# Kernel tuning notes

Measured on AMD Instinct MI355X. Metric: run time of the kernel, lower is better.

Reference implementation:

```python
import jax, jax.numpy as jnp
import numpy as np

SEQ = 8192
IN_DIM = 1024
HIDDEN_DIM = 2048
N_EXPERTS = 8
TOPK = 2


def setup_inputs() -> dict:
    key = jax.random.key(0)
    ks = jax.random.split(key, 6)
    scale = 0.02
    inp = jax.random.normal(ks[0], (SEQ, IN_DIM), jnp.float32)
    weights = jax.random.uniform(ks[1], (SEQ, TOPK), jnp.float32)
    selections = jax.random.randint(ks[2], (SEQ, TOPK), 0, N_EXPERTS, jnp.int32)
    up_proj = jax.random.normal(ks[3], (HIDDEN_DIM * N_EXPERTS, IN_DIM), jnp.float32) * scale
    gate_proj = jax.random.normal(ks[4], (HIDDEN_DIM * N_EXPERTS, IN_DIM), jnp.float32) * scale
    down_proj = jax.random.normal(ks[5], (HIDDEN_DIM * N_EXPERTS, IN_DIM), jnp.float32) * scale
    return {"inp": inp, "weights": weights, "up_proj": up_proj,
            "gate_proj": gate_proj, "down_proj": down_proj, "selections": selections}


def reference(inp, weights, up_proj, gate_proj, down_proj, selections):
    seq, in_dim = inp.shape
    topk = selections.shape[-1]
    # dispatch: replicate each token topk times -> (seq*topk, in_dim)
    x = jnp.broadcast_to(inp[:, None, :], (seq, topk, in_dim)).reshape(-1, in_dim)
    e_ids = selections.reshape(-1)  # (seq*topk,) expert id per dispatched token
    W_up = up_proj.reshape(N_EXPERTS, HIDDEN_DIM, in_dim)
    W_gate = gate_proj.reshape(N_EXPERTS, HIDDEN_DIM, in_dim)
    W_down = down_proj.reshape(N_EXPERTS, HIDDEN_DIM, in_dim)
    out = jnp.zeros_like(x)
    # grouped (block-sparse) GEMM: loop over the small fixed expert set,
    # masking tokens not routed to this expert (gelu(0)*0 = 0, so math matches).
    for e in range(N_EXPERTS):
        mask = (e_ids == e)[:, None]
        xe = jnp.where(mask, x, 0.0)
        h = xe @ W_up[e].T        # (seq*topk, hidden)
        g = xe @ W_gate[e].T      # (seq*topk, hidden)
        out = out + jnp.where(mask, (jax.nn.gelu(g) * h) @ W_down[e], 0.0)
    # combine: weighted sum over topk expert outputs per token
    return (out.reshape(seq, topk, in_dim) * weights[:, :, None]).sum(axis=1)
```

## Files before the change

kernel.cpp:

```cpp
#include <hip/hip_runtime.h>


#define SEQ 8192
#define IN_DIM 1024
#define HID 2048
#define NEXP 8
#define TOPK 2
#define NSLOT (SEQ * TOPK)

#define BM 128
#define BK 64
#define MAX_TILES 136
#define BM1 256
#define MAX_T1 72

typedef unsigned short ushort_t;
typedef __bf16 bf16x8 __attribute__((ext_vector_type(8)));
typedef float f32x4 __attribute__((ext_vector_type(4)));

__device__ __forceinline__ ushort_t f2bf(float f) {
    union { float f; unsigned u; } v;
    v.f = f;
    unsigned r = v.u + 0x7FFFu + ((v.u >> 16) & 1u);
    return (ushort_t)(r >> 16);
}

__device__ __forceinline__ float gelu_tanh(float x) {
    float u = 0.7978845608028654f * x * (1.0f + 0.044715f * x * x);
    return x / (1.0f + __expf(-2.0f * u));
}

__device__ __forceinline__ void async16(const void* g, void* l) {
    __builtin_amdgcn_global_load_lds(
        (const __attribute__((address_space(1))) unsigned int*)g,
        (__attribute__((address_space(3))) unsigned int*)l, 16, 0, 0);
}

__device__ __forceinline__ void wait8_barrier() {
    asm volatile("s_waitcnt vmcnt(8)\ns_barrier" ::: "memory");
}
__device__ __forceinline__ void wait0_barrier() {
    asm volatile("s_waitcnt vmcnt(0)\ns_barrier" ::: "memory");
}
__device__ __forceinline__ void lds_barrier() {
    asm volatile("s_waitcnt lgkmcnt(0)\ns_barrier" ::: "memory");
}

__global__ void cast_bf16_kernel(const float* __restrict__ in,
                                 ushort_t* __restrict__ out, int n) {
    int i = (blockIdx.x * blockDim.x + threadIdx.x) * 4;
    if (i >= n) return;
    float4 v = *(const float4*)(in + i);
    union { ushort_t u[4]; uint2 v; } o;
    o.u[0] = f2bf(v.x); o.u[1] = f2bf(v.y);
    o.u[2] = f2bf(v.z); o.u[3] = f2bf(v.w);
    *(uint2*)(out + i) = o.v;
}

__global__ void transpose_cast_kernel(const float* __restrict__ in,
                                      ushort_t* __restrict__ out) {
    __shared__ float tile[32][33];
    int e = blockIdx.z;
    int d0 = blockIdx.x * 32, h0 = blockIdx.y * 32;
    int tx = threadIdx.x & 31, ty = threadIdx.x >> 5;
    const float* src = in + (size_t)e * HID * IN_DIM;
    for (int j = 0; j < 32; j += 8)
        tile[ty + j][tx] = src[(size_t)(h0 + ty + j) * IN_DIM + d0 + tx];
    __syncthreads();
    ushort_t* dst = out + (size_t)e * IN_DIM * HID;
    for (int j = 0; j < 32; j += 8)
        dst[(size_t)(d0 + ty + j) * HID + h0 + tx] = f2bf(tile[tx][ty + j]);
}

__global__ void route_kernel(const int* __restrict__ sel,
                             const float* __restrict__ wts,
                             int* __restrict__ meta,
                             int* __restrict__ stok,
                             int* __restrict__ sinv) {
    __shared__ int lc[256][NEXP];
    __shared__ int tot[NEXP];
    __shared__ int s_off[NEXP + 1];
    int t = threadIdx.x;
    int cnt[NEXP];
#pragma unroll
    for (int e = 0; e < NEXP; e++) cnt[e] = 0;
    int base = t * (NSLOT / 256);
    for (int i = 0; i < NSLOT / 256; i++) cnt[sel[base + i]]++;
#pragma unroll
    for (int e = 0; e < NEXP; e++) lc[t][e] = cnt[e];
    __syncthreads();
    if (t < NEXP) {
        int run = 0;
        for (int i = 0; i < 256; i++) { int v = lc[i][t]; lc[i][t] = run; run += v; }
        tot[t] = run;
    }
    __syncthreads();
    if (t == 0) {
        int o = 0;
        for (int e = 0; e < NEXP; e++) { s_off[e] = o; o += tot[e]; }
        s_off[NEXP] = o;
        for (int e = 0; e <= NEXP; e++) meta[e] = s_off[e];
        int nt = 0;
        for (int e = 0; e < NEXP; e++) {
            int c = s_off[e + 1] - s_off[e];
            int m = (c + BM - 1) / BM;
            for (int i = 0; i < m; i++) { meta[32 + 2 * nt] = e; meta[33 + 2 * nt] = i; nt++; }
        }
        meta[16] = nt;
    }
    __syncthreads();
    int cur[NEXP];
#pragma unroll
    for (int e = 0; e < NEXP; e++) cur[e] = s_off[e] + lc[t][e];
    for (int i = 0; i < NSLOT / 256; i++) {
        int slot = base + i;
        int e = sel[slot];
        int pos = cur[e]++;
        stok[pos] = slot >> 1;
        sinv[slot] = pos;
    }
}

__global__ __launch_bounds__(512, 2) void gemm1_kernel(
    const ushort_t* __restrict__ X,
    const ushort_t* __restrict__ U,
    const ushort_t* __restrict__ G,
    const int* __restrict__ meta,
    const int* __restrict__ stok,
    ushort_t* __restrict__ act) {
    __shared__ __align__(16) ushort_t AT[2][2][128 * BK];
    __shared__ __align__(16) ushort_t UT[2][128 * BK];
    __shared__ __align__(16) ushort_t GT[2][128 * BK];
    __shared__ int s_tok[BM1];

    int tile = blockIdx.x;
    int e = -1, mt = 0, accT = 0;
#pragma unroll
    for (int ee = 0; ee < NEXP; ee++) {
        int c = meta[ee + 1] - meta[ee];
        int m = (c + BM1 - 1) >> 8;
        if (tile >= accT && tile < accT + m) { e = ee; mt = tile - accT; }
        accT += m;
    }
    if (e < 0) return;
    int off = meta[e];
    int cnt = meta[e + 1] - off;
    int m0 = mt * BM1;
    int n0 = blockIdx.y * 128;

    int tid = threadIdx.x;
    if (tid < BM1) {
        int r = m0 + tid;
        if (r >= cnt) r = cnt - 1;
        s_tok[tid] = stok[off + r];
    }
    __syncthreads();

    int lane = tid & 63;
    int w = tid >> 6;
    int wm = w >> 2;
    int wn = w & 3;
    int srow = lane >> 3;
    int schunk = lane & 7;
    int gchunk = schunk ^ srow;
    int r4 = lane & 15;
    int q = lane >> 4;
    int sw7 = r4 & 7;

    const ushort_t* Xp[2][2];
#pragma unroll
    for (int h = 0; h < 2; h++)
#pragma unroll
        for (int j = 0; j < 2; j++) {
            int r = h * 128 + w * 16 + j * 8 + srow;
            Xp[h][j] = X + (size_t)s_tok[r] * IN_DIM + gchunk * 8;
        }
    const ushort_t* Ue = U + ((size_t)e * HID + n0) * IN_DIM;
    const ushort_t* Ge = G + ((size_t)e * HID + n0) * IN_DIM;
    const ushort_t* Upt[2];
    const ushort_t* Gpt[2];
#pragma unroll
    for (int j = 0; j < 2; j++) {
        int r = w * 16 + j * 8 + srow;
        Upt[j] = Ue + (size_t)r * IN_DIM + gchunk * 8;
        Gpt[j] = Ge + (size_t)r * IN_DIM + gchunk * 8;
    }

    f32x4 accH[8][2], accG[8][2];
#pragma unroll
    for (int mi = 0; mi < 8; mi++)
#pragma unroll
        for (int ni = 0; ni < 2; ni++) {
            accH[mi][ni] = (f32x4){0.f, 0.f, 0.f, 0.f};
            accG[mi][ni] = (f32x4){0.f, 0.f, 0.f, 0.f};
        }

    bf16x8 a[4][2], bu[2][2], bg[2][2];

#define ST_A(b, h, kt) {                                                   \
        async16(Xp[h][0] + (kt), &AT[b][h][(w * 16) * BK]);                \
        async16(Xp[h][1] + (kt), &AT[b][h][(w * 16 + 8) * BK]); }
#define ST_U(b, kt) {                                                      \
        async16(Upt[0] + (kt), &UT[b][(w * 16) * BK]);                     \
        async16(Upt[1] + (kt), &UT[b][(w * 16 + 8) * BK]); }
#define ST_G(b, kt) {                                                      \
        async16(Gpt[0] + (kt), &GT[b][(w * 16) * BK]);                     \
        async16(Gpt[1] + (kt), &GT[b][(w * 16 + 8) * BK]); }

#define RD_A(b, mb) {                                                      \
        _Pragma("unroll") for (int mi = 0; mi < 4; mi++)                   \
        _Pragma("unroll") for (int kh = 0; kh < 2; kh++)                   \
            a[mi][kh] = *(const bf16x8*)&AT[b][wm][                        \
                ((mb) + mi * 16 + r4) * BK + (((kh * 4 + q) ^ sw7) << 3)]; }
#define RD_U(b) {                                                          \
        _Pragma("unroll") for (int ni = 0; ni < 2; ni++)                   \
        _Pragma("unroll") for (int kh = 0; kh < 2; kh++)                   \
            bu[ni][kh] = *(const bf16x8*)&UT[b][                           \
                (wn * 32 + ni * 16 + r4) * BK + (((kh * 4 + q) ^ sw7) << 3)]; }
#define RD_G(b) {                                                          \
        _Pragma("unroll") for (int ni = 0; ni < 2; ni++)                   \
        _Pragma("unroll") for (int kh = 0; kh < 2; kh++)                   \
            bg[ni][kh] = *(const bf16x8*)&GT[b][                           \
                (wn * 32 + ni * 16 + r4) * BK + (((kh * 4 + q) ^ sw7) << 3)]; }

#define MM(ACC, mb2, BB) {                                                 \
        _Pragma("unroll") for (int mi = 0; mi < 4; mi++)                   \
        _Pragma("unroll") for (int ni = 0; ni < 2; ni++)                   \
        _Pragma("unroll") for (int kh = 0; kh < 2; kh++)                   \
            ACC[(mb2) + mi][ni] = __builtin_amdgcn_mfma_f32_16x16x32_bf16( \
                a[mi][kh], BB[ni][kh], ACC[(mb2) + mi][ni], 0, 0, 0); }

#define BARRIER __builtin_amdgcn_s_barrier()
#define LGKM0 asm volatile("s_waitcnt lgkmcnt(0)" ::: "memory")
#define VMW2 asm volatile("s_waitcnt vmcnt(2)" ::: "memory")
#define PRIO1 __builtin_amdgcn_s_setprio(1)
#define PRIO0 __builtin_amdgcn_s_setprio(0)

    ST_A(0, 0, 0); ST_A(0, 1, 0); ST_U(0, 0); ST_G(0, 0);
    ST_A(1, 0, BK);
    VMW2; BARRIER;

    for (int it = 0; it < 8; it++) {
        int t = 2 * it;
        int k1 = (t + 1) * BK;
        int k2 = (t + 2 < 16 ? t + 2 : 15) * BK;
        int k3 = (t + 3 < 16 ? t + 3 : 15) * BK;
        RD_A(0, 0); RD_U(0);
        ST_A(1, 1, k1);
        BARRIER; LGKM0;
        PRIO1; MM(accH, 0, bu); PRIO0; BARRIER;
        RD_G(0);
        ST_U(1, k1);
        BARRIER; LGKM0;
        PRIO1; MM(accG, 0, bg); PRIO0; BARRIER;
        RD_A(0, 64);
        ST_G(1, k1);
        BARRIER; LGKM0;
        PRIO1; MM(accG, 4, bg); PRIO0; BARRIER;
        ST_A(0, 0, k2);
        VMW2; BARRIER;
        PRIO1; MM(accH, 4, bu); PRIO0; BARRIER;
        RD_A(1, 0); RD_U(1);
        ST_A(0, 1, k2);
        BARRIER; LGKM0;
        PRIO1; MM(accH, 0, bu); PRIO0; BARRIER;
        RD_G(1);
        ST_U(0, k2);
        BARRIER; LGKM0;
        PRIO1; MM(accG, 0, bg); PRIO0; BARRIER;
        RD_A(1, 64);
        ST_G(0, k2);
        BARRIER; LGKM0;
        PRIO1; MM(accG, 4, bg); PRIO0; BARRIER;
        ST_A(1, 0, k3);
        VMW2; BARRIER;
        PRIO1; MM(accH, 4, bu); PRIO0; BARRIER;
    }

#pragma unroll
    for (int mf = 0; mf < 8; mf++) {
#pragma unroll
        for (int r = 0; r < 4; r++) {
            int row_local = wm * 128 + mf * 16 + q * 4 + r;
            int grow = m0 + row_local;
            if (grow >= cnt) continue;
            size_t orow = (size_t)(off + grow) * HID + n0 + wn * 32;
#pragma unroll
            for (int ni = 0; ni < 2; ni++) {
                float h = accH[mf][ni][r];
                float g = accG[mf][ni][r];
                act[orow + ni * 16 + r4] = f2bf(gelu_tanh(g) * h);
            }
        }
    }
#undef ST_A
#undef ST_U
#undef ST_G
#undef RD_A
#undef RD_U
#undef RD_G
#undef MM
}

__global__ __launch_bounds__(256) void gemm2_kernel(
    const ushort_t* __restrict__ act,
    const ushort_t* __restrict__ DT,
    const int* __restrict__ meta,
    float* __restrict__ y) {
    __shared__ __align__(16) ushort_t AT[2][BM * BK];
    __shared__ __align__(16) ushort_t BT[2][BM * BK];

    int tile = blockIdx.x;
    if (tile >= meta[16]) return;
    int e = meta[32 + 2 * tile];
    int mt = meta[33 + 2 * tile];
    int off = meta[e];
    int cnt = meta[e + 1] - off;
    int m0 = mt * BM;
    int n0 = blockIdx.y * 128;

    int tid = threadIdx.x;
    int lane = tid & 63;
    int w = tid >> 6;
    int wr = w >> 1, wc = w & 1;
    int srow = lane >> 3;
    int schunk = lane & 7;
    int gchunk = schunk ^ srow;

    const ushort_t* Ae = act + (size_t)off * HID;
    const ushort_t* Be = DT + ((size_t)e * IN_DIM + n0) * HID;

    const ushort_t* ap[4];
    const ushort_t* bp[4];
#pragma unroll
    for (int i = 0; i < 4; i++) {
        int r = w * 32 + i * 8 + srow;
        int ar = m0 + r; if (ar >= cnt) ar = cnt - 1;
        ap[i] = Ae + (size_t)ar * HID + gchunk * 8;
        bp[i] = Be + (size_t)r * HID + gchunk * 8;
    }

    f32x4 acc[4][4];
#pragma unroll
    for (int mi = 0; mi < 4; mi++)
#pragma unroll
        for (int ni = 0; ni < 4; ni++) acc[mi][ni] = (f32x4){0.f, 0.f, 0.f, 0.f};

    int r4 = lane & 15;
    int q = lane >> 4;
    int sw7 = r4 & 7;

#define G2_ISSUE(s)                                                        \
    {                                                                      \
        int _b = (s) & 1;                                                  \
        int _k0 = (s) * BK;                                                \
        _Pragma("unroll")                                                  \
        for (int i = 0; i < 4; i++) {                                      \
            async16(ap[i] + _k0, &AT[_b][(w * 32 + i * 8) * BK]);          \
            async16(bp[i] + _k0, &BT[_b][(w * 32 + i * 8) * BK]);          \
        }                                                                  \
    }

#define G2_COMPUTE(s)                                                      \
    {                                                                      \
        int _b = (s) & 1;                                                  \
        _Pragma("unroll")                                                  \
        for (int kk = 0; kk < BK; kk += 32) {                              \
            int c = (kk >> 3) + q;                                         \
            int cs = ((c ^ sw7) << 3);                                     \
            bf16x8 a[4], b[4];                                             \
            _Pragma("unroll")                                              \
            for (int i = 0; i < 4; i++) {                                  \
                a[i] = *(const bf16x8*)&AT[_b][(wr * 64 + i * 16 + r4) * BK + cs]; \
                b[i] = *(const bf16x8*)&BT[_b][(wc * 64 + i * 16 + r4) * BK + cs]; \
            }                                                              \
            _Pragma("unroll")                                              \
            for (int mi = 0; mi < 4; mi++)                                 \
                _Pragma("unroll")                                          \
                for (int ni = 0; ni < 4; ni++)                             \
                    acc[mi][ni] = __builtin_amdgcn_mfma_f32_16x16x32_bf16( \
                        a[mi], b[ni], acc[mi][ni], 0, 0, 0);               \
        }                                                                  \
    }

    const int NK = HID / BK;
    G2_ISSUE(0);
    for (int s = 0; s < NK - 1; s++) {
        G2_ISSUE(s + 1);
        wait8_barrier();
        G2_COMPUTE(s);
        lds_barrier();
    }
    wait0_barrier();
    G2_COMPUTE(NK - 1);

#pragma unroll
    for (int mi = 0; mi < 4; mi++) {
#pragma unroll
        for (int r = 0; r < 4; r++) {
            int row_local = wr * 64 + mi * 16 + q * 4 + r;
            int grow = m0 + row_local;
            if (grow >= cnt) continue;
            float* orow = y + (size_t)(off + grow) * IN_DIM + n0 + wc * 64;
#pragma unroll
            for (int ni = 0; ni < 4; ni++)
                orow[ni * 16 + r4] = acc[mi][ni][r];
        }
    }
}

__global__ __launch_bounds__(256) void combine_kernel(
    const float* __restrict__ y,
    const float* __restrict__ wts,
    const int* __restrict__ sinv,
    float* __restrict__ out) {
    int tok = blockIdx.x;
    int c = threadIdx.x;
    int p0 = sinv[tok * 2], p1 = sinv[tok * 2 + 1];
    float w0 = wts[tok * 2], w1 = wts[tok * 2 + 1];
    float4 a = *(const float4*)(y + (size_t)p0 * IN_DIM + c * 4);
    float4 b = *(const float4*)(y + (size_t)p1 * IN_DIM + c * 4);
    float4 o;
    o.x = w0 * a.x + w1 * b.x;
    o.y = w0 * a.y + w1 * b.y;
    o.z = w0 * a.z + w1 * b.z;
    o.w = w0 * a.w + w1 * b.w;
    *(float4*)(out + (size_t)tok * IN_DIM + c * 4) = o;
}

extern "C" void kernel_launch(void* const* d_in, const int* in_sizes, int n_in,
                              void* d_out, int out_size, void* d_ws, size_t ws_size,
                              hipStream_t stream) {
    const float* inp  = (const float*)d_in[0];
    const float* wts  = (const float*)d_in[1];
    const float* up   = (const float*)d_in[2];
    const float* gate = (const float*)d_in[3];
    const float* down = (const float*)d_in[4];
    const int*   sel  = (const int*)d_in[5];
    float* out = (float*)d_out;

    char* ws = (char*)d_ws;
    ushort_t* inp_bf  = (ushort_t*)(ws);
    ushort_t* up_bf   = (ushort_t*)(ws + 16777216);
    ushort_t* gate_bf = (ushort_t*)(ws + 50331648);
    ushort_t* down_bf = (ushort_t*)(ws + 83886080);
    ushort_t* act     = (ushort_t*)(ws + 117440512);
    int*      stok    = (int*)(ws + 184549376);
    int*      sinv    = (int*)(ws + 184614912);
    int*      meta    = (int*)(ws + 184680448);
    float*    y       = (float*)(ws);

    cast_bf16_kernel<<<(SEQ * IN_DIM) / 1024, 256, 0, stream>>>(inp, inp_bf, SEQ * IN_DIM);
    cast_bf16_kernel<<<(NEXP * HID * IN_DIM) / 1024, 256, 0, stream>>>(up, up_bf, NEXP * HID * IN_DIM);
    cast_bf16_kernel<<<(NEXP * HID * IN_DIM) / 1024, 256, 0, stream>>>(gate, gate_bf, NEXP * HID * IN_DIM);
    transpose_cast_kernel<<<dim3(IN_DIM / 32, HID / 32, NEXP), 256, 0, stream>>>(down, down_bf);
    route_kernel<<<1, 256, 0, stream>>>(sel, wts, meta, stok, sinv);
    gemm1_kernel<<<dim3(MAX_T1, HID / 128), 512, 0, stream>>>(inp_bf, up_bf, gate_bf, meta, stok, act);
    gemm2_kernel<<<dim3(MAX_TILES, IN_DIM / 128), 256, 0, stream>>>(act, down_bf, meta, y);
    combine_kernel<<<SEQ, 256, 0, stream>>>(y, wts, sinv, out);
}
```

Before: 573.2 us.

## Reuse gemm1's 256x256 pipelined schedule for gemm2 and remap tile order

Rewrites the down-projection GEMM so it runs the same 512-thread, 256-row software-pipelined schedule as gemm1, treating two 128-column halves of the output as the U/G operands. This gives 256x256 tiles in place of 128x128 with a simple double buffer. Both GEMMs also get a block-id swizzle that groups tiles sharing the same weight panel, and the k-loop becomes a pointer-advancing non-unrolled loop with a peeled tail. The aim is more operand reuse and better cache locality, at the cost of fewer blocks and higher register and LDS pressure in gemm2.

```diff
diff --git a/kernel.cpp b/kernel.cpp
--- a/kernel.cpp
+++ b/kernel.cpp
@@ -10,7 +10,6 @@
 
 #define BM 128
 #define BK 64
-#define MAX_TILES 136
 #define BM1 256
 #define MAX_T1 72
 
@@ -34,16 +33,6 @@
     __builtin_amdgcn_global_load_lds(
         (const __attribute__((address_space(1))) unsigned int*)g,
         (__attribute__((address_space(3))) unsigned int*)l, 16, 0, 0);
-}
-
-__device__ __forceinline__ void wait8_barrier() {
-    asm volatile("s_waitcnt vmcnt(8)\ns_barrier" ::: "memory");
-}
-__device__ __forceinline__ void wait0_barrier() {
-    asm volatile("s_waitcnt vmcnt(0)\ns_barrier" ::: "memory");
-}
-__device__ __forceinline__ void lds_barrier() {
-    asm volatile("s_waitcnt lgkmcnt(0)\ns_barrier" ::: "memory");
 }
 
 __global__ void cast_bf16_kernel(const float* __restrict__ in,
@@ -121,91 +110,15 @@
     }
 }
 
-__global__ __launch_bounds__(512, 2) void gemm1_kernel(
-    const ushort_t* __restrict__ X,
-    const ushort_t* __restrict__ U,
-    const ushort_t* __restrict__ G,
-    const int* __restrict__ meta,
-    const int* __restrict__ stok,
-    ushort_t* __restrict__ act) {
-    __shared__ __align__(16) ushort_t AT[2][2][128 * BK];
-    __shared__ __align__(16) ushort_t UT[2][128 * BK];
-    __shared__ __align__(16) ushort_t GT[2][128 * BK];
-    __shared__ int s_tok[BM1];
-
-    int tile = blockIdx.x;
-    int e = -1, mt = 0, accT = 0;
-#pragma unroll
-    for (int ee = 0; ee < NEXP; ee++) {
-        int c = meta[ee + 1] - meta[ee];
-        int m = (c + BM1 - 1) >> 8;
-        if (tile >= accT && tile < accT + m) { e = ee; mt = tile - accT; }
-        accT += m;
-    }
-    if (e < 0) return;
-    int off = meta[e];
-    int cnt = meta[e + 1] - off;
-    int m0 = mt * BM1;
-    int n0 = blockIdx.y * 128;
-
-    int tid = threadIdx.x;
-    if (tid < BM1) {
-        int r = m0 + tid;
-        if (r >= cnt) r = cnt - 1;
-        s_tok[tid] = stok[off + r];
-    }
-    __syncthreads();
-
-    int lane = tid & 63;
-    int w = tid >> 6;
-    int wm = w >> 2;
-    int wn = w & 3;
-    int srow = lane >> 3;
-    int schunk = lane & 7;
-    int gchunk = schunk ^ srow;
-    int r4 = lane & 15;
-    int q = lane >> 4;
-    int sw7 = r4 & 7;
-
-    const ushort_t* Xp[2][2];
-#pragma unroll
-    for (int h = 0; h < 2; h++)
-#pragma unroll
-        for (int j = 0; j < 2; j++) {
-            int r = h * 128 + w * 16 + j * 8 + srow;
-            Xp[h][j] = X + (size_t)s_tok[r] * IN_DIM + gchunk * 8;
-        }
-    const ushort_t* Ue = U + ((size_t)e * HID + n0) * IN_DIM;
-    const ushort_t* Ge = G + ((size_t)e * HID + n0) * IN_DIM;
-    const ushort_t* Upt[2];
-    const ushort_t* Gpt[2];
-#pragma unroll
-    for (int j = 0; j < 2; j++) {
-        int r = w * 16 + j * 8 + srow;
-        Upt[j] = Ue + (size_t)r * IN_DIM + gchunk * 8;
-        Gpt[j] = Ge + (size_t)r * IN_DIM + gchunk * 8;
-    }
-
-    f32x4 accH[8][2], accG[8][2];
-#pragma unroll
-    for (int mi = 0; mi < 8; mi++)
-#pragma unroll
-        for (int ni = 0; ni < 2; ni++) {
-            accH[mi][ni] = (f32x4){0.f, 0.f, 0.f, 0.f};
-            accG[mi][ni] = (f32x4){0.f, 0.f, 0.f, 0.f};
-        }
-
-    bf16x8 a[4][2], bu[2][2], bg[2][2];
-
-#define ST_A(b, h, kt) {                                                   \
-        async16(Xp[h][0] + (kt), &AT[b][h][(w * 16) * BK]);                \
-        async16(Xp[h][1] + (kt), &AT[b][h][(w * 16 + 8) * BK]); }
-#define ST_U(b, kt) {                                                      \
-        async16(Upt[0] + (kt), &UT[b][(w * 16) * BK]);                     \
-        async16(Upt[1] + (kt), &UT[b][(w * 16 + 8) * BK]); }
-#define ST_G(b, kt) {                                                      \
-        async16(Gpt[0] + (kt), &GT[b][(w * 16) * BK]);                     \
-        async16(Gpt[1] + (kt), &GT[b][(w * 16 + 8) * BK]); }
+#define ST_A(b, h, koff) {                                                 \
+        async16(pA[h][0] + (koff), &AT[b][h][(w * 16) * BK]);              \
+        async16(pA[h][1] + (koff), &AT[b][h][(w * 16 + 8) * BK]); }
+#define ST_U(b, koff) {                                                    \
+        async16(pU[0] + (koff), &UT[b][(w * 16) * BK]);                    \
+        async16(pU[1] + (koff), &UT[b][(w * 16 + 8) * BK]); }
+#define ST_G(b, koff) {                                                    \
+        async16(pG[0] + (koff), &GT[b][(w * 16) * BK]);                    \
+        async16(pG[1] + (koff), &GT[b][(w * 16 + 8) * BK]); }
 
 #define RD_A(b, mb) {                                                      \
         _Pragma("unroll") for (int mi = 0; mi < 4; mi++)                   \
@@ -233,49 +146,143 @@
 #define BARRIER __builtin_amdgcn_s_barrier()
 #define LGKM0 asm volatile("s_waitcnt lgkmcnt(0)" ::: "memory")
 #define VMW2 asm volatile("s_waitcnt vmcnt(2)" ::: "memory")
+#define VMW0 asm volatile("s_waitcnt vmcnt(0)" ::: "memory")
 #define PRIO1 __builtin_amdgcn_s_setprio(1)
 #define PRIO0 __builtin_amdgcn_s_setprio(0)
 
-    ST_A(0, 0, 0); ST_A(0, 1, 0); ST_U(0, 0); ST_G(0, 0);
-    ST_A(1, 0, BK);
+#define KPRO                                                               \
+    ST_A(0, 0, 0); ST_A(0, 1, 0); ST_U(0, 0); ST_G(0, 0);                  \
+    ST_A(1, 0, 64);                                                        \
     VMW2; BARRIER;
 
-    for (int it = 0; it < 8; it++) {
-        int t = 2 * it;
-        int k1 = (t + 1) * BK;
-        int k2 = (t + 2 < 16 ? t + 2 : 15) * BK;
-        int k3 = (t + 3 < 16 ? t + 3 : 15) * BK;
-        RD_A(0, 0); RD_U(0);
-        ST_A(1, 1, k1);
-        BARRIER; LGKM0;
-        PRIO1; MM(accH, 0, bu); PRIO0; BARRIER;
-        RD_G(0);
-        ST_U(1, k1);
-        BARRIER; LGKM0;
-        PRIO1; MM(accG, 0, bg); PRIO0; BARRIER;
-        RD_A(0, 64);
-        ST_G(1, k1);
-        BARRIER; LGKM0;
-        PRIO1; MM(accG, 4, bg); PRIO0; BARRIER;
-        ST_A(0, 0, k2);
-        VMW2; BARRIER;
-        PRIO1; MM(accH, 4, bu); PRIO0; BARRIER;
-        RD_A(1, 0); RD_U(1);
-        ST_A(0, 1, k2);
-        BARRIER; LGKM0;
-        PRIO1; MM(accH, 0, bu); PRIO0; BARRIER;
-        RD_G(1);
-        ST_U(0, k2);
-        BARRIER; LGKM0;
-        PRIO1; MM(accG, 0, bg); PRIO0; BARRIER;
-        RD_A(1, 64);
-        ST_G(0, k2);
-        BARRIER; LGKM0;
-        PRIO1; MM(accG, 4, bg); PRIO0; BARRIER;
-        ST_A(1, 0, k3);
-        VMW2; BARRIER;
-        PRIO1; MM(accH, 4, bu); PRIO0; BARRIER;
-    }
+#define KBODY_FULL                                                         \
+    RD_A(0, 0); RD_U(0); ST_A(1, 1, 64); BARRIER; LGKM0;                   \
+    PRIO1; MM(accH, 0, bu); PRIO0; BARRIER;                                \
+    RD_G(0); ST_U(1, 64); BARRIER; LGKM0;                                  \
+    PRIO1; MM(accG, 0, bg); PRIO0; BARRIER;                                \
+    RD_A(0, 64); ST_G(1, 64); BARRIER; LGKM0;                              \
+    PRIO1; MM(accG, 4, bg); PRIO0; BARRIER;                                \
+    ST_A(0, 0, 128); VMW2; BARRIER;                                        \
+    PRIO1; MM(accH, 4, bu); PRIO0; BARRIER;                                \
+    RD_A(1, 0); RD_U(1); ST_A(0, 1, 128); BARRIER; LGKM0;                  \
+    PRIO1; MM(accH, 0, bu); PRIO0; BARRIER;                                \
+    RD_G(1); ST_U(0, 128); BARRIER; LGKM0;                                 \
+    PRIO1; MM(accG, 0, bg); PRIO0; BARRIER;                                \
+    RD_A(1, 64); ST_G(0, 128); BARRIER; LGKM0;                             \
+    PRIO1; MM(accG, 4, bg); PRIO0; BARRIER;                                \
+    ST_A(1, 0, 192); VMW2; BARRIER;                                        \
+    PRIO1; MM(accH, 4, bu); PRIO0; BARRIER;
+
+#define KBODY_ADV {                                                        \
+    pA[0][0] += 128; pA[0][1] += 128; pA[1][0] += 128; pA[1][1] += 128;    \
+    pU[0] += 128; pU[1] += 128; pG[0] += 128; pG[1] += 128; }
+
+#define KBODY_TAIL                                                         \
+    RD_A(0, 0); RD_U(0); ST_A(1, 1, 64); BARRIER; LGKM0;                   \
+    PRIO1; MM(accH, 0, bu); PRIO0; BARRIER;                                \
+    RD_G(0); ST_U(1, 64); BARRIER; LGKM0;                                  \
+    PRIO1; MM(accG, 0, bg); PRIO0; BARRIER;                                \
+    RD_A(0, 64); ST_G(1, 64); BARRIER; LGKM0;                              \
+    PRIO1; MM(accG, 4, bg); PRIO0; BARRIER;                                \
+    VMW0; BARRIER;                                                         \
+    PRIO1; MM(accH, 4, bu); PRIO0; BARRIER;                                \
+    RD_A(1, 0); RD_U(1); BARRIER; LGKM0;                                   \
+    PRIO1; MM(accH, 0, bu); PRIO0; BARRIER;                                \
+    RD_G(1); BARRIER; LGKM0;                                               \
+    PRIO1; MM(accG, 0, bg); PRIO0; BARRIER;                                \
+    RD_A(1, 64); BARRIER; LGKM0;                                           \
+    PRIO1; MM(accG, 4, bg); PRIO0; BARRIER;                                \
+    PRIO1; MM(accH, 4, bu); PRIO0;
+
+#define TILE_DERIVE(tile)                                                  \
+    int e = -1, mt = 0, accT = 0;                                          \
+    _Pragma("unroll")                                                      \
+    for (int ee = 0; ee < NEXP; ee++) {                                    \
+        int c = meta[ee + 1] - meta[ee];                                   \
+        int m = (c + BM1 - 1) >> 8;                                        \
+        if ((tile) >= accT && (tile) < accT + m) { e = ee; mt = (tile) - accT; } \
+        accT += m;                                                         \
+    }                                                                      \
+    if (e < 0) return;                                                     \
+    int off = meta[e];                                                     \
+    int cnt = meta[e + 1] - off;                                           \
+    int m0 = mt * BM1;
+
+__global__ __launch_bounds__(512, 2) void gemm1_kernel(
+    const ushort_t* __restrict__ X,
+    const ushort_t* __restrict__ U,
+    const ushort_t* __restrict__ G,
+    const int* __restrict__ meta,
+    const int* __restrict__ stok,
+    ushort_t* __restrict__ act) {
+    __shared__ __align__(16) ushort_t AT[2][2][128 * BK];
+    __shared__ __align__(16) ushort_t UT[2][128 * BK];
+    __shared__ __align__(16) ushort_t GT[2][128 * BK];
+    __shared__ int s_tok[BM1];
+
+    int id = blockIdx.x + MAX_T1 * blockIdx.y;
+    int wi = (id & 7) * 144 + (id >> 3);
+    int tile = wi % MAX_T1;
+    int n0 = (wi / MAX_T1) * 128;
+
+    TILE_DERIVE(tile);
+
+    int tid = threadIdx.x;
+    if (tid < BM1) {
+        int r = m0 + tid;
+        if (r >= cnt) r = cnt - 1;
+        s_tok[tid] = stok[off + r];
+    }
+    __syncthreads();
+
+    int lane = tid & 63;
+    int w = tid >> 6;
+    int wm = w >> 2;
+    int wn = w & 3;
+    int srow = lane >> 3;
+    int schunk = lane & 7;
+    int gchunk = schunk ^ srow;
+    int r4 = lane & 15;
+    int q = lane >> 4;
+    int sw7 = r4 & 7;
+
+    const ushort_t* pA[2][2];
+#pragma unroll
+    for (int h = 0; h < 2; h++)
+#pragma unroll
+        for (int j = 0; j < 2; j++) {
+            int r = h * 128 + w * 16 + j * 8 + srow;
+            pA[h][j] = X + (size_t)s_tok[r] * IN_DIM + gchunk * 8;
+        }
+    const ushort_t* Ue = U + ((size_t)e * HID + n0) * IN_DIM;
+    const ushort_t* Ge = G + ((size_t)e * HID + n0) * IN_DIM;
+    const ushort_t* pU[2];
+    const ushort_t* pG[2];
+#pragma unroll
+    for (int j = 0; j < 2; j++) {
+        int r = w * 16 + j * 8 + srow;
+        pU[j] = Ue + (size_t)r * IN_DIM + gchunk * 8;
+        pG[j] = Ge + (size_t)r * IN_DIM + gchunk * 8;
+    }
+
+    f32x4 accH[8][2], accG[8][2];
+#pragma unroll
+    for (int mi = 0; mi < 8; mi++)
+#pragma unroll
+        for (int ni = 0; ni < 2; ni++) {
+            accH[mi][ni] = (f32x4){0.f, 0.f, 0.f, 0.f};
+            accG[mi][ni] = (f32x4){0.f, 0.f, 0.f, 0.f};
+        }
+
+    bf16x8 a[4][2], bu[2][2], bg[2][2];
+
+    KPRO;
+#pragma unroll 1
+    for (int i = 0; i < (IN_DIM / BK) / 2 - 1; ++i) {
+        KBODY_FULL;
+        KBODY_ADV;
+    }
+    KBODY_TAIL;
 
 #pragma unroll
     for (int mf = 0; mf < 8; mf++) {
@@ -293,118 +300,88 @@
             }
         }
     }
-#undef ST_A
-#undef ST_U
-#undef ST_G
-#undef RD_A
-#undef RD_U
-#undef RD_G
-#undef MM
-}
-
-__global__ __launch_bounds__(256) void gemm2_kernel(
+}
+
+__global__ __launch_bounds__(512, 2) void gemm2_kernel(
     const ushort_t* __restrict__ act,
     const ushort_t* __restrict__ DT,
     const int* __restrict__ meta,
     float* __restrict__ y) {
-    __shared__ __align__(16) ushort_t AT[2][BM * BK];
-    __shared__ __align__(16) ushort_t BT[2][BM * BK];
-
-    int tile = blockIdx.x;
-    if (tile >= meta[16]) return;
-    int e = meta[32 + 2 * tile];
-    int mt = meta[33 + 2 * tile];
-    int off = meta[e];
-    int cnt = meta[e + 1] - off;
-    int m0 = mt * BM;
-    int n0 = blockIdx.y * 128;
+    __shared__ __align__(16) ushort_t AT[2][2][128 * BK];
+    __shared__ __align__(16) ushort_t UT[2][128 * BK];
+    __shared__ __align__(16) ushort_t GT[2][128 * BK];
+
+    int id = blockIdx.x + MAX_T1 * blockIdx.y;
+    int wi = (id & 7) * 36 + (id >> 3);
+    int tile = wi % MAX_T1;
+    int n0 = (wi / MAX_T1) * 256;
+
+    TILE_DERIVE(tile);
 
     int tid = threadIdx.x;
     int lane = tid & 63;
     int w = tid >> 6;
-    int wr = w >> 1, wc = w & 1;
+    int wm = w >> 2;
+    int wn = w & 3;
     int srow = lane >> 3;
     int schunk = lane & 7;
     int gchunk = schunk ^ srow;
-
-    const ushort_t* Ae = act + (size_t)off * HID;
-    const ushort_t* Be = DT + ((size_t)e * IN_DIM + n0) * HID;
-
-    const ushort_t* ap[4];
-    const ushort_t* bp[4];
-#pragma unroll
-    for (int i = 0; i < 4; i++) {
-        int r = w * 32 + i * 8 + srow;
-        int ar = m0 + r; if (ar >= cnt) ar = cnt - 1;
-        ap[i] = Ae + (size_t)ar * HID + gchunk * 8;
-        bp[i] = Be + (size_t)r * HID + gchunk * 8;
-    }
-
-    f32x4 acc[4][4];
-#pragma unroll
-    for (int mi = 0; mi < 4; mi++)
-#pragma unroll
-        for (int ni = 0; ni < 4; ni++) acc[mi][ni] = (f32x4){0.f, 0.f, 0.f, 0.f};
-
     int r4 = lane & 15;
     int q = lane >> 4;
     int sw7 = r4 & 7;
 
-#define G2_ISSUE(s)                                                        \
-    {                                                                      \
-        int _b = (s) & 1;                                                  \
-        int _k0 = (s) * BK;                                                \
-        _Pragma("unroll")                                                  \
-        for (int i = 0; i < 4; i++) {                                      \
-            async16(ap[i] + _k0, &AT[_b][(w * 32 + i * 8) * BK]);          \
-            async16(bp[i] + _k0, &BT[_b][(w * 32 + i * 8) * BK]);          \
-        }                                                                  \
-    }
-
-#define G2_COMPUTE(s)                                                      \
-    {                                                                      \
-        int _b = (s) & 1;                                                  \
-        _Pragma("unroll")                                                  \
-        for (int kk = 0; kk < BK; kk += 32) {                              \
-            int c = (kk >> 3) + q;                                         \
-            int cs = ((c ^ sw7) << 3);                                     \
-            bf16x8 a[4], b[4];                                             \
-            _Pragma("unroll")                                              \
-            for (int i = 0; i < 4; i++) {                                  \
-                a[i] = *(const bf16x8*)&AT[_b][(wr * 64 + i * 16 + r4) * BK + cs]; \
-                b[i] = *(const bf16x8*)&BT[_b][(wc * 64 + i * 16 + r4) * BK + cs]; \
-            }                                                              \
-            _Pragma("unroll")                                              \
-            for (int mi = 0; mi < 4; mi++)                                 \
-                _Pragma("unroll")                                          \
-                for (int ni = 0; ni < 4; ni++)                             \
-                    acc[mi][ni] = __builtin_amdgcn_mfma_f32_16x16x32_bf16( \
-                        a[mi], b[ni], acc[mi][ni], 0, 0, 0);               \
-        }                                                                  \
-    }
-
-    const int NK = HID / BK;
-    G2_ISSUE(0);
-    for (int s = 0; s < NK - 1; s++) {
-        G2_ISSUE(s + 1);
-        wait8_barrier();
-        G2_COMPUTE(s);
-        lds_barrier();
-    }
-    wait0_barrier();
-    G2_COMPUTE(NK - 1);
-
-#pragma unroll
-    for (int mi = 0; mi < 4; mi++) {
+    const ushort_t* Ae = act + (size_t)off * HID;
+    const ushort_t* pA[2][2];
+#pragma unroll
+    for (int h = 0; h < 2; h++)
+#pragma unroll
+        for (int j = 0; j < 2; j++) {
+            int ar = m0 + h * 128 + w * 16 + j * 8 + srow;
+            if (ar >= cnt) ar = cnt - 1;
+            pA[h][j] = Ae + (size_t)ar * HID + gchunk * 8;
+        }
+    const ushort_t* Be = DT + ((size_t)e * IN_DIM + n0) * HID;
+    const ushort_t* pU[2];
+    const ushort_t* pG[2];
+#pragma unroll
+    for (int j = 0; j < 2; j++) {
+        int r = w * 16 + j * 8 + srow;
+        pU[j] = Be + (size_t)r * HID + gchunk * 8;
+        pG[j] = Be + (size_t)(128 + r) * HID + gchunk * 8;
+    }
+
+    f32x4 accH[8][2], accG[8][2];
+#pragma unroll
+    for (int mi = 0; mi < 8; mi++)
+#pragma unroll
+        for (int ni = 0; ni < 2; ni++) {
+            accH[mi][ni] = (f32x4){0.f, 0.f, 0.f, 0.f};
+            accG[mi][ni] = (f32x4){0.f, 0.f, 0.f, 0.f};
+        }
+
+    bf16x8 a[4][2], bu[2][2], bg[2][2];
+
+    KPRO;
+#pragma unroll 1
+    for (int i = 0; i < (HID / BK) / 2 - 1; ++i) {
+        KBODY_FULL;
+        KBODY_ADV;
+    }
+    KBODY_TAIL;
+
+#pragma unroll
+    for (int mf = 0; mf < 8; mf++) {
 #pragma unroll
         for (int r = 0; r < 4; r++) {
-            int row_local = wr * 64 + mi * 16 + q * 4 + r;
+            int row_local = wm * 128 + mf * 16 + q * 4 + r;
             int grow = m0 + row_local;
             if (grow >= cnt) continue;
-            float* orow = y + (size_t)(off + grow) * IN_DIM + n0 + wc * 64;
-#pragma unroll
-            for (int ni = 0; ni < 4; ni++)
-                orow[ni * 16 + r4] = acc[mi][ni][r];
+            float* orow = y + (size_t)(off + grow) * IN_DIM + n0 + wn * 32;
+#pragma unroll
+            for (int ni = 0; ni < 2; ni++) {
+                orow[ni * 16 + r4] = accH[mf][ni][r];
+                orow[128 + ni * 16 + r4] = accG[mf][ni][r];
+            }
         }
     }
 }
@@ -456,6 +433,6 @@
     transpose_cast_kernel<<<dim3(IN_DIM / 32, HID / 32, NEXP), 256, 0, stream>>>(down, down_bf);
     route_kernel<<<1, 256, 0, stream>>>(sel, wts, meta, stok, sinv);
     gemm1_kernel<<<dim3(MAX_T1, HID / 128), 512, 0, stream>>>(inp_bf, up_bf, gate_bf, meta, stok, act);
-    gemm2_kernel<<<dim3(MAX_TILES, IN_DIM / 128), 256, 0, stream>>>(act, down_bf, meta, y);
+    gemm2_kernel<<<dim3(MAX_T1, IN_DIM / 256), 512, 0, stream>>>(act, down_bf, meta, y);
     combine_kernel<<<SEQ, 256, 0, stream>>>(y, wts, sinv, out);
 }
```

Measured after the change: 567.1 us. About the same (-1.1%).
